# Kernel optimization log

Measured on AMD Instinct MI355X. Metric: run time of the kernel, lower is better.

## Reference

```python
import jax, jax.numpy as jnp
import numpy as np

HEADS = 8  # head_dim = 512 // 8 = 64


def setup_inputs() -> dict:
    key = jax.random.key(0)
    ks = jax.random.split(key, 6)
    B, S, D = 1, 4096, 512
    s = 0.02
    return {
        "hidden_states": jax.random.normal(ks[0], (B, S, D), dtype=jnp.float32),
        "Wq": jax.random.normal(ks[1], (D, D), dtype=jnp.float32) * s,
        "Wk": jax.random.normal(ks[2], (D, D), dtype=jnp.float32) * s,
        "Wv": jax.random.normal(ks[3], (D, D), dtype=jnp.float32) * s,
        "Wo": jax.random.normal(ks[4], (D, D), dtype=jnp.float32) * s,
        "b_out": jnp.zeros((D,), dtype=jnp.float32),
    }


def reference(hidden_states, Wq, Wk, Wv, Wo, b_out):
    B, S, D = hidden_states.shape
    H = HEADS
    hd = D // H
    scale = 1.0 / jnp.sqrt(jnp.asarray(hd, hidden_states.dtype))

    # unfused QKV projections (self-attention, no mask)
    q = hidden_states @ Wq  # [B,S,D]
    k = hidden_states @ Wk
    v = hidden_states @ Wv

    # head_to_batch_dim: [B,S,D] -> [B,H,S,hd]
    def split_heads(t):
        return t.reshape(B, S, H, hd).transpose(0, 2, 1, 3)

    q, k, v = split_heads(q), split_heads(k), split_heads(v)

    # explicit score matrix + softmax (faithful to torch.bmm path)
    scores = jnp.einsum("bhqd,bhkd->bhqk", q, k) * scale  # [B,H,S,S]
    probs = jax.nn.softmax(scores, axis=-1)
    out = jnp.einsum("bhqk,bhkd->bhqd", probs, v)  # [B,H,S,hd]

    # batch_to_head_dim: [B,H,S,hd] -> [B,S,D]
    out = out.transpose(0, 2, 1, 3).reshape(B, S, D)
    # to_out[0] Linear + to_out[1] Dropout (identity at eval)
    return out @ Wo + b_out
```

## Files before the change

kernel.cpp:

```cpp
#include <hip/hip_runtime.h>
#include <hip/hip_bf16.h>

#define S_LEN 4096
#define DMODEL 512
#define NHEADS 8
#define HDIM 64

typedef __hip_bfloat16 bf16;
typedef __attribute__((ext_vector_type(8))) short bf16x8;
typedef __attribute__((ext_vector_type(4))) float f32x4;
typedef __attribute__((ext_vector_type(2))) _Float16 f16x2;
typedef __attribute__((ext_vector_type(4))) _Float16 f16x4;
typedef __attribute__((ext_vector_type(8))) _Float16 f16x8;

__device__ __forceinline__ f32x4 mfma16x16x32(bf16x8 a, bf16x8 b, f32x4 c) {
    return __builtin_amdgcn_mfma_f32_16x16x32_bf16(a, b, c, 0, 0, 0);
}
__device__ __forceinline__ f32x4 mfma16x16x32h(f16x8 a, f16x8 b, f32x4 c) {
    return __builtin_amdgcn_mfma_f32_16x16x32_f16(a, b, c, 0, 0, 0);
}
__device__ __forceinline__ void gload_lds16(const void* g, void* l) {
    __builtin_amdgcn_global_load_lds(
        (const __attribute__((address_space(1))) unsigned int*)g,
        (__attribute__((address_space(3))) unsigned int*)l, 16, 0, 0);
}

__global__ __launch_bounds__(256) void prep(
    const float* __restrict__ X,
    const float* __restrict__ Wq, const float* __restrict__ Wk,
    const float* __restrict__ Wv, const float* __restrict__ Wo,
    bf16* __restrict__ Xb, bf16* __restrict__ Wt)
{
    __shared__ bf16 tile[32][33];
    const int b = blockIdx.x;
    if (b < 1024) {
        int i = (b * 256 + threadIdx.x) * 8;
        float4 a = *(const float4*)(X + i);
        float4 c = *(const float4*)(X + i + 4);
        bf16 tmp[8];
        tmp[0] = __float2bfloat16(a.x); tmp[1] = __float2bfloat16(a.y);
        tmp[2] = __float2bfloat16(a.z); tmp[3] = __float2bfloat16(a.w);
        tmp[4] = __float2bfloat16(c.x); tmp[5] = __float2bfloat16(c.y);
        tmp[6] = __float2bfloat16(c.z); tmp[7] = __float2bfloat16(c.w);
        *(bf16x8*)(Xb + i) = *(bf16x8*)tmp;
    } else {
        const int bb = b - 1024;
        const int z = bb >> 8;
        const int bx = bb & 15, by = (bb >> 4) & 15;
        const float* src = (z == 0) ? Wq : (z == 1) ? Wk : (z == 2) ? Wv : Wo;
        bf16* dst = Wt + (size_t)z * DMODEL * DMODEL;
        const int tx = threadIdx.x & 31, ty = threadIdx.x >> 5;
        const int x = bx * 32 + tx;
        const int y0 = by * 32;
        #pragma unroll
        for (int i = ty; i < 32; i += 8)
            tile[i][tx] = __float2bfloat16(src[(size_t)(y0 + i) * DMODEL + x]);
        __syncthreads();
        const int xo = y0 + tx;
        #pragma unroll
        for (int i = ty; i < 32; i += 8)
            dst[(size_t)(bx * 32 + i) * DMODEL + xo] = tile[tx][i];
    }
}

__global__ __launch_bounds__(256) void gemm_qkv(
    const bf16* __restrict__ A, const bf16* __restrict__ Bt,
    bf16* __restrict__ Qm, bf16* __restrict__ Km, _Float16* __restrict__ Vt)
{
    __shared__ __align__(16) char smem[65536];
    const int m0 = blockIdx.x * 64, n0 = blockIdx.y * 64;
    const int t = threadIdx.x, lane = t & 63, w = t >> 6;
    const int lr = lane & 15, lq = lane >> 4;
    const int swz = (lr & 7) << 4;

    f32x4 acc[3][4];
    #pragma unroll
    for (int i = 0; i < 3; ++i)
        #pragma unroll
        for (int n = 0; n < 4; ++n) acc[i][n] = f32x4{0, 0, 0, 0};

    const int srow = w * 8 + (lane >> 3);
    const int scol = ((lane & 7) ^ (lane >> 3)) * 8;
    const bf16* Ab = A + (size_t)(m0 + srow) * DMODEL + scol;
    const bf16* Bb = Bt + (size_t)(n0 + srow) * DMODEL + scol;

#define QKV_STAGE(k0, b) do {                                                  \
        char* ad = smem + (b) * 8192 + w * 1024;                               \
        gload_lds16(Ab + (k0), ad);                                            \
        gload_lds16(Ab + 32 * DMODEL + (k0), ad + 4096);                       \
        _Pragma("unroll")                                                      \
        for (int mat = 0; mat < 3; ++mat) {                                    \
            char* bd = smem + 16384 + ((b) * 3 + mat) * 8192 + w * 1024;       \
            gload_lds16(Bb + mat * DMODEL * DMODEL + (k0), bd);                \
            gload_lds16(Bb + mat * DMODEL * DMODEL + 32 * DMODEL + (k0), bd + 4096); \
        }                                                                      \
    } while (0)

    QKV_STAGE(0, 0);
    #pragma unroll
    for (int ks = 0; ks < 8; ++ks) {
        const int cur = ks & 1;
        if (ks < 7) {
            QKV_STAGE((ks + 1) * 64, cur ^ 1);
            asm volatile("s_waitcnt vmcnt(8)" ::: "memory");
        } else {
            asm volatile("s_waitcnt vmcnt(0)" ::: "memory");
        }
        __builtin_amdgcn_s_barrier();
        __builtin_amdgcn_sched_barrier(0);
        #pragma unroll
        for (int kc = 0; kc < 2; ++kc) {
            const int co = (kc * 64 + lq * 16) ^ swz;
            bf16x8 a = *(const bf16x8*)(smem + cur * 8192 + (w * 16 + lr) * 128 + co);
            #pragma unroll
            for (int mat = 0; mat < 3; ++mat)
                #pragma unroll
                for (int nt = 0; nt < 4; ++nt) {
                    bf16x8 b = *(const bf16x8*)(smem + 16384 + (cur * 3 + mat) * 8192 +
                                                (nt * 16 + lr) * 128 + co);
                    acc[mat][nt] = mfma16x16x32(a, b, acc[mat][nt]);
                }
        }
        asm volatile("s_waitcnt lgkmcnt(0)" ::: "memory");
        __builtin_amdgcn_sched_barrier(0);
        __builtin_amdgcn_s_barrier();
    }
#undef QKV_STAGE

    bf16*     tbq = (bf16*)smem;
    bf16*     tbk = (bf16*)(smem + 9216);
    _Float16* tbv = (_Float16*)(smem + 18432);
    #pragma unroll
    for (int nt = 0; nt < 4; ++nt)
        #pragma unroll
        for (int r = 0; r < 4; ++r) {
            int row = w * 16 + lq * 4 + r, col = nt * 16 + lr;
            tbq[row * 72 + col] = __float2bfloat16(acc[0][nt][r] * 0.18033688f);
            tbk[row * 72 + col] = __float2bfloat16(acc[1][nt][r]);
            tbv[row * 72 + col] = (_Float16)acc[2][nt][r];
        }
    __syncthreads();
    #pragma unroll
    for (int pass = 0; pass < 2; ++pass) {
        const int m = pass * 32 + (t >> 3), c0 = (t & 7) * 8;
        *(bf16x8*)(Qm + (size_t)(m0 + m) * DMODEL + n0 + c0) =
            *(const bf16x8*)(tbq + m * 72 + c0);
        *(bf16x8*)(Km + (size_t)(m0 + m) * DMODEL + n0 + c0) =
            *(const bf16x8*)(tbk + m * 72 + c0);
    }
    {
        const int c = t >> 2, seg = t & 3;
        _Float16 tmp[16];
        #pragma unroll
        for (int j = 0; j < 16; ++j)
            tmp[j] = tbv[(seg * 16 + j) * 72 + c];
        _Float16* vp = Vt + (size_t)(n0 + c) * S_LEN + m0;
        #pragma unroll
        for (int g = 0; g < 4; ++g) {
            f16x4 vv = {tmp[g * 4 + 0], tmp[g * 4 + 1], tmp[g * 4 + 2], tmp[g * 4 + 3]};
            *(f16x4*)(vp + g * 16 + seg * 4) = vv;
        }
    }
}

__global__ __launch_bounds__(256) void gemm_out(
    const bf16* __restrict__ A, const bf16* __restrict__ Bt,
    float* __restrict__ Out, const float* __restrict__ bias)
{
    __shared__ __align__(16) char smem[32768];
    const int m0 = blockIdx.x * 64, n0 = blockIdx.y * 64;
    const int t = threadIdx.x, lane = t & 63, w = t >> 6;
    const int lr = lane & 15, lq = lane >> 4;
    const int swz = (lr & 7) << 4;

    f32x4 acc[4] = {f32x4{0,0,0,0}, f32x4{0,0,0,0}, f32x4{0,0,0,0}, f32x4{0,0,0,0}};

    const int srow = w * 8 + (lane >> 3);
    const int scol = ((lane & 7) ^ (lane >> 3)) * 8;
    const bf16* Ab = A + (size_t)(m0 + srow) * DMODEL + scol;
    const bf16* Bb = Bt + (size_t)(n0 + srow) * DMODEL + scol;

#define OUT_STAGE(k0, b) do {                                           \
        char* ad = smem + (b) * 8192 + w * 1024;                        \
        char* bd = smem + 16384 + (b) * 8192 + w * 1024;                \
        gload_lds16(Ab + (k0), ad);                                     \
        gload_lds16(Ab + 32 * DMODEL + (k0), ad + 4096);                \
        gload_lds16(Bb + (k0), bd);                                     \
        gload_lds16(Bb + 32 * DMODEL + (k0), bd + 4096);                \
    } while (0)

    OUT_STAGE(0, 0);
    #pragma unroll
    for (int ks = 0; ks < 8; ++ks) {
        const int cur = ks & 1;
        if (ks < 7) {
            OUT_STAGE((ks + 1) * 64, cur ^ 1);
            asm volatile("s_waitcnt vmcnt(4)" ::: "memory");
        } else {
            asm volatile("s_waitcnt vmcnt(0)" ::: "memory");
        }
        __builtin_amdgcn_s_barrier();
        __builtin_amdgcn_sched_barrier(0);
        #pragma unroll
        for (int kc = 0; kc < 2; ++kc) {
            const int co = (kc * 64 + lq * 16) ^ swz;
            bf16x8 a = *(const bf16x8*)(smem + cur * 8192 + (w * 16 + lr) * 128 + co);
            #pragma unroll
            for (int nt = 0; nt < 4; ++nt) {
                bf16x8 b = *(const bf16x8*)(smem + 16384 + cur * 8192 + (nt * 16 + lr) * 128 + co);
                acc[nt] = mfma16x16x32(a, b, acc[nt]);
            }
        }
        asm volatile("s_waitcnt lgkmcnt(0)" ::: "memory");
        __builtin_amdgcn_sched_barrier(0);
        __builtin_amdgcn_s_barrier();
    }
#undef OUT_STAGE

    float* tb = (float*)smem;
    #pragma unroll
    for (int nt = 0; nt < 4; ++nt) {
        const float bv = bias[n0 + nt * 16 + lr];
        #pragma unroll
        for (int r = 0; r < 4; ++r)
            tb[(w * 16 + lq * 4 + r) * 68 + nt * 16 + lr] = acc[nt][r] + bv;
    }
    __syncthreads();
    #pragma unroll
    for (int pass = 0; pass < 2; ++pass) {
        const int m = pass * 32 + (t >> 3), c0 = (t & 7) * 8;
        float4 v0 = *(const float4*)(tb + m * 68 + c0);
        float4 v1 = *(const float4*)(tb + m * 68 + c0 + 4);
        *(float4*)(Out + (size_t)(m0 + m) * DMODEL + n0 + c0) = v0;
        *(float4*)(Out + (size_t)(m0 + m) * DMODEL + n0 + c0 + 4) = v1;
    }
}

__global__ __launch_bounds__(256, 2) void attn_kernel(
    const bf16* __restrict__ Q, const bf16* __restrict__ Kmat,
    const _Float16* __restrict__ Vt, bf16* __restrict__ Oout)
{
    __shared__ __align__(16) char smem[65536];

    const int h = blockIdx.x, qb = blockIdx.y;
    const int t = threadIdx.x, lane = t & 63, w = t >> 6;
    const int lr = lane & 15, lq = lane >> 4;
    const int q0 = qb * 64;

    char* myK = smem + w * 16384;
    char* myV = myK + 8192;

    const int sr = lane >> 3;
    const int scc = (lane & 7) ^ sr;
    const bf16*     gK = Kmat + (size_t)sr * DMODEL + h * HDIM + scc * 8;
    const _Float16* gV = Vt + (size_t)(h * HDIM + sr) * S_LEN + scc * 8;

    bf16x8 qf[4][2];
    #pragma unroll
    for (int qt = 0; qt < 4; ++qt) {
        const bf16* qp = Q + (size_t)(q0 + qt * 16 + lr) * DMODEL + h * HDIM + lq * 8;
        qf[qt][0] = *(const bf16x8*)qp;
        qf[qt][1] = *(const bf16x8*)(qp + 32);
    }

    f32x4 oacc[4][4];
    #pragma unroll
    for (int i = 0; i < 4; ++i)
        #pragma unroll
        for (int j = 0; j < 4; ++j) oacc[i][j] = f32x4{0, 0, 0, 0};
    f32x4 lacc[4];
    #pragma unroll
    for (int i = 0; i < 4; ++i) lacc[i] = f32x4{0, 0, 0, 0};
    const f16x8 vones = {(_Float16)1.0f, (_Float16)1.0f, (_Float16)1.0f, (_Float16)1.0f,
                         (_Float16)1.0f, (_Float16)1.0f, (_Float16)1.0f, (_Float16)1.0f};

    #pragma unroll
    for (int i = 0; i < 8; ++i) {
        gload_lds16(gK + (size_t)(w * 64 + i * 8) * DMODEL, myK + i * 1024);
        gload_lds16(gV + (size_t)(i * 8) * S_LEN + w * 64, myV + i * 1024);
    }

    const int swz = (lr & 7) << 4;

    for (int kt = w; kt < S_LEN / 64; kt += 4) {
        asm volatile("s_waitcnt vmcnt(0)" ::: "memory");

        bf16x8 kf[4][2];
        #pragma unroll
        for (int mt = 0; mt < 4; ++mt) {
            const char* kr = myK + (mt * 16 + lr) * 128;
            kf[mt][0] = *(const bf16x8*)(kr + ((lq * 16) ^ swz));
            kf[mt][1] = *(const bf16x8*)(kr + ((64 + lq * 16) ^ swz));
        }
        f16x8 vA[4], vB[4];
        #pragma unroll
        for (int ht = 0; ht < 4; ++ht) {
            const char* vr = myV + (ht * 16 + lr) * 128;
            vA[ht] = *(const f16x8*)(vr + ((lq * 32) ^ swz));
            vB[ht] = *(const f16x8*)(vr + ((lq * 32 + 16) ^ swz));
        }
        asm volatile("s_waitcnt lgkmcnt(0)" ::: "memory");
        __builtin_amdgcn_sched_barrier(0);

        const int ktn = kt + 4;
        if (ktn < S_LEN / 64) {
            #pragma unroll
            for (int i = 0; i < 8; ++i) {
                gload_lds16(gK + (size_t)(ktn * 64 + i * 8) * DMODEL, myK + i * 1024);
                gload_lds16(gV + (size_t)(i * 8) * S_LEN + ktn * 64, myV + i * 1024);
            }
        }

        __builtin_amdgcn_s_setprio(1);
        f16x4 pf[4][4];
        #pragma unroll
        for (int qt = 0; qt < 4; ++qt) {
            f32x4 st[4];
            #pragma unroll
            for (int mt = 0; mt < 4; ++mt) {
                f32x4 z = {0, 0, 0, 0};
                z = mfma16x16x32(kf[mt][0], qf[qt][0], z);
                z = mfma16x16x32(kf[mt][1], qf[qt][1], z);
                st[mt] = z;
            }
            #pragma unroll
            for (int mt = 0; mt < 4; ++mt) {
                float p0 = __builtin_amdgcn_exp2f(st[mt][0]);
                float p1 = __builtin_amdgcn_exp2f(st[mt][1]);
                float p2 = __builtin_amdgcn_exp2f(st[mt][2]);
                float p3 = __builtin_amdgcn_exp2f(st[mt][3]);
                f16x2 c01 = __builtin_bit_cast(f16x2, __builtin_amdgcn_cvt_pkrtz(p0, p1));
                f16x2 c23 = __builtin_bit_cast(f16x2, __builtin_amdgcn_cvt_pkrtz(p2, p3));
                pf[qt][mt] = __builtin_shufflevector(c01, c23, 0, 1, 2, 3);
            }
        }
        #pragma unroll
        for (int qt = 0; qt < 4; ++qt) {
            f16x8 pp01 = __builtin_shufflevector(pf[qt][0], pf[qt][1], 0, 1, 2, 3, 4, 5, 6, 7);
            f16x8 pp23 = __builtin_shufflevector(pf[qt][2], pf[qt][3], 0, 1, 2, 3, 4, 5, 6, 7);
            #pragma unroll
            for (int ht = 0; ht < 4; ++ht) {
                oacc[qt][ht] = mfma16x16x32h(pp01, vA[ht], oacc[qt][ht]);
                oacc[qt][ht] = mfma16x16x32h(pp23, vB[ht], oacc[qt][ht]);
            }
            lacc[qt] = mfma16x16x32h(pp01, vones, lacc[qt]);
            lacc[qt] = mfma16x16x32h(pp23, vones, lacc[qt]);
        }
        __builtin_amdgcn_s_setprio(0);
    }

    __syncthreads();
    float (*obuf)[3][4][64][4] = (float(*)[3][4][64][4])smem;
    float (*lbuf)[4][16]       = (float(*)[4][16])(smem + 49152);

    #pragma unroll
    for (int qt = 0; qt < 4; ++qt) {
        if (qt != w) {
            int j = qt - (qt > w ? 1 : 0);
            #pragma unroll
            for (int ht = 0; ht < 4; ++ht)
                *(f32x4*)&obuf[w][j][ht][lane][0] = oacc[qt][ht];
        }
    }
    if (lr == 0) {
        #pragma unroll
        for (int qt = 0; qt < 4; ++qt)
            #pragma unroll
            for (int r = 0; r < 4; ++r)
                lbuf[w][qt][lq * 4 + r] = lacc[qt][r];
    }
    __syncthreads();

    f32x4 osum[4];
    #pragma unroll
    for (int qt = 0; qt < 4; ++qt)
        if (qt == w) {
            #pragma unroll
            for (int ht = 0; ht < 4; ++ht) osum[ht] = oacc[qt][ht];
        }
    #pragma unroll
    for (int w2 = 0; w2 < 4; ++w2) {
        if (w2 == w) continue;
        int j = w - (w > w2 ? 1 : 0);
        #pragma unroll
        for (int ht = 0; ht < 4; ++ht)
            osum[ht] += *(const f32x4*)&obuf[w2][j][ht][lane][0];
    }
    float linv[4];
    #pragma unroll
    for (int r = 0; r < 4; ++r) {
        int rr = lq * 4 + r;
        linv[r] = 1.0f / (lbuf[0][w][rr] + lbuf[1][w][rr] + lbuf[2][w][rr] + lbuf[3][w][rr]);
    }
    #pragma unroll
    for (int r = 0; r < 4; ++r) {
        int row = q0 + w * 16 + lq * 4 + r;
        #pragma unroll
        for (int ht = 0; ht < 4; ++ht)
            Oout[(size_t)row * DMODEL + h * HDIM + ht * 16 + lr] =
                __float2bfloat16(osum[ht][r] * linv[r]);
    }
}

extern "C" void kernel_launch(void* const* d_in, const int* in_sizes, int n_in,
                              void* d_out, int out_size, void* d_ws, size_t ws_size,
                              hipStream_t stream) {
    const float* X  = (const float*)d_in[0];
    const float* Wq = (const float*)d_in[1];
    const float* Wk = (const float*)d_in[2];
    const float* Wv = (const float*)d_in[3];
    const float* Wo = (const float*)d_in[4];
    const float* bo = (const float*)d_in[5];
    float* out = (float*)d_out;

    char* ws = (char*)d_ws;
    bf16* Wt = (bf16*)ws;
    bf16* Xb = (bf16*)(ws + (size_t)4 * DMODEL * DMODEL * 2);
    bf16* Qm = Xb + (size_t)S_LEN * DMODEL;
    bf16* Km = Qm + (size_t)S_LEN * DMODEL;
    _Float16* Vt = (_Float16*)(Km + (size_t)S_LEN * DMODEL);
    bf16* AO = (bf16*)(Vt + (size_t)S_LEN * DMODEL);

    bf16* Wot = Wt + (size_t)3 * DMODEL * DMODEL;

    prep<<<2048, 256, 0, stream>>>(X, Wq, Wk, Wv, Wo, Xb, Wt);

    gemm_qkv<<<dim3(S_LEN / 64, DMODEL / 64), 256, 0, stream>>>(
        Xb, Wt, Qm, Km, Vt);

    attn_kernel<<<dim3(NHEADS, S_LEN / 64), 256, 0, stream>>>(Qm, Km, Vt, AO);

    gemm_out<<<dim3(S_LEN / 64, DMODEL / 64), 256, 0, stream>>>(AO, Wot, out, bo);
}
```

Before: 126.7 us.

## Split attention q-tiles across wave pairs sharing K/V LDS staging

The attention block grows from 4 to 8 waves. Each pair of waves shares one K/V LDS buffer, with only the first four waves issuing the global-to-LDS loads. Each wave now handles 2 query tiles instead of 4, which cuts accumulator register pressure and allows more resident waves per CU. The cost is two s_barriers per iteration to coordinate staging and reuse of the shared buffers. The final reduction is reorganized so that each half of the waves combines its partial sums and softmax denominators in LDS.

Measured after the change: 152.6 us. +20.4%, slower.

```diff
diff --git a/kernel.cpp b/kernel.cpp
--- a/kernel.cpp
+++ b/kernel.cpp
@@ -236,7 +236,7 @@
     }
 }
 
-__global__ __launch_bounds__(256, 2) void attn_kernel(
+__global__ __launch_bounds__(512, 4) void attn_kernel(
     const bf16* __restrict__ Q, const bf16* __restrict__ Kmat,
     const _Float16* __restrict__ Vt, bf16* __restrict__ Oout)
 {
@@ -246,8 +246,11 @@
     const int t = threadIdx.x, lane = t & 63, w = t >> 6;
     const int lr = lane & 15, lq = lane >> 4;
     const int q0 = qb * 64;
-
-    char* myK = smem + w * 16384;
+    const int p = w & 3;
+    const bool stager = (w < 4);
+    const int qtbase = stager ? 0 : 2;
+
+    char* myK = smem + p * 16384;
     char* myV = myK + 8192;
 
     const int sr = lane >> 3;
@@ -255,35 +258,38 @@
     const bf16*     gK = Kmat + (size_t)sr * DMODEL + h * HDIM + scc * 8;
     const _Float16* gV = Vt + (size_t)(h * HDIM + sr) * S_LEN + scc * 8;
 
-    bf16x8 qf[4][2];
-    #pragma unroll
-    for (int qt = 0; qt < 4; ++qt) {
-        const bf16* qp = Q + (size_t)(q0 + qt * 16 + lr) * DMODEL + h * HDIM + lq * 8;
-        qf[qt][0] = *(const bf16x8*)qp;
-        qf[qt][1] = *(const bf16x8*)(qp + 32);
-    }
-
-    f32x4 oacc[4][4];
-    #pragma unroll
-    for (int i = 0; i < 4; ++i)
+    bf16x8 qf[2][2];
+    #pragma unroll
+    for (int ql = 0; ql < 2; ++ql) {
+        const bf16* qp = Q + (size_t)(q0 + (qtbase + ql) * 16 + lr) * DMODEL + h * HDIM + lq * 8;
+        qf[ql][0] = *(const bf16x8*)qp;
+        qf[ql][1] = *(const bf16x8*)(qp + 32);
+    }
+
+    f32x4 oacc[2][4];
+    #pragma unroll
+    for (int i = 0; i < 2; ++i)
         #pragma unroll
         for (int j = 0; j < 4; ++j) oacc[i][j] = f32x4{0, 0, 0, 0};
-    f32x4 lacc[4];
-    #pragma unroll
-    for (int i = 0; i < 4; ++i) lacc[i] = f32x4{0, 0, 0, 0};
+    f32x4 lacc[2];
+    lacc[0] = f32x4{0, 0, 0, 0};
+    lacc[1] = f32x4{0, 0, 0, 0};
     const f16x8 vones = {(_Float16)1.0f, (_Float16)1.0f, (_Float16)1.0f, (_Float16)1.0f,
                          (_Float16)1.0f, (_Float16)1.0f, (_Float16)1.0f, (_Float16)1.0f};
 
-    #pragma unroll
-    for (int i = 0; i < 8; ++i) {
-        gload_lds16(gK + (size_t)(w * 64 + i * 8) * DMODEL, myK + i * 1024);
-        gload_lds16(gV + (size_t)(i * 8) * S_LEN + w * 64, myV + i * 1024);
+    if (stager) {
+        #pragma unroll
+        for (int i = 0; i < 8; ++i) {
+            gload_lds16(gK + (size_t)(p * 64 + i * 8) * DMODEL, myK + i * 1024);
+            gload_lds16(gV + (size_t)(i * 8) * S_LEN + p * 64, myV + i * 1024);
+        }
     }
 
     const int swz = (lr & 7) << 4;
 
-    for (int kt = w; kt < S_LEN / 64; kt += 4) {
-        asm volatile("s_waitcnt vmcnt(0)" ::: "memory");
+    for (int kt = p; kt < S_LEN / 64; kt += 4) {
+        if (stager) asm volatile("s_waitcnt vmcnt(0)" ::: "memory");
+        __builtin_amdgcn_s_barrier();
 
         bf16x8 kf[4][2];
         #pragma unroll
@@ -292,35 +298,16 @@
             kf[mt][0] = *(const bf16x8*)(kr + ((lq * 16) ^ swz));
             kf[mt][1] = *(const bf16x8*)(kr + ((64 + lq * 16) ^ swz));
         }
-        f16x8 vA[4], vB[4];
-        #pragma unroll
-        for (int ht = 0; ht < 4; ++ht) {
-            const char* vr = myV + (ht * 16 + lr) * 128;
-            vA[ht] = *(const f16x8*)(vr + ((lq * 32) ^ swz));
-            vB[ht] = *(const f16x8*)(vr + ((lq * 32 + 16) ^ swz));
-        }
-        asm volatile("s_waitcnt lgkmcnt(0)" ::: "memory");
-        __builtin_amdgcn_sched_barrier(0);
-
-        const int ktn = kt + 4;
-        if (ktn < S_LEN / 64) {
-            #pragma unroll
-            for (int i = 0; i < 8; ++i) {
-                gload_lds16(gK + (size_t)(ktn * 64 + i * 8) * DMODEL, myK + i * 1024);
-                gload_lds16(gV + (size_t)(i * 8) * S_LEN + ktn * 64, myV + i * 1024);
-            }
-        }
-
-        __builtin_amdgcn_s_setprio(1);
-        f16x4 pf[4][4];
-        #pragma unroll
-        for (int qt = 0; qt < 4; ++qt) {
+
+        f16x4 pf[2][4];
+        #pragma unroll
+        for (int ql = 0; ql < 2; ++ql) {
             f32x4 st[4];
             #pragma unroll
             for (int mt = 0; mt < 4; ++mt) {
                 f32x4 z = {0, 0, 0, 0};
-                z = mfma16x16x32(kf[mt][0], qf[qt][0], z);
-                z = mfma16x16x32(kf[mt][1], qf[qt][1], z);
+                z = mfma16x16x32(kf[mt][0], qf[ql][0], z);
+                z = mfma16x16x32(kf[mt][1], qf[ql][1], z);
                 st[mt] = z;
             }
             #pragma unroll
@@ -331,74 +318,97 @@
                 float p3 = __builtin_amdgcn_exp2f(st[mt][3]);
                 f16x2 c01 = __builtin_bit_cast(f16x2, __builtin_amdgcn_cvt_pkrtz(p0, p1));
                 f16x2 c23 = __builtin_bit_cast(f16x2, __builtin_amdgcn_cvt_pkrtz(p2, p3));
-                pf[qt][mt] = __builtin_shufflevector(c01, c23, 0, 1, 2, 3);
+                pf[ql][mt] = __builtin_shufflevector(c01, c23, 0, 1, 2, 3);
             }
         }
-        #pragma unroll
-        for (int qt = 0; qt < 4; ++qt) {
-            f16x8 pp01 = __builtin_shufflevector(pf[qt][0], pf[qt][1], 0, 1, 2, 3, 4, 5, 6, 7);
-            f16x8 pp23 = __builtin_shufflevector(pf[qt][2], pf[qt][3], 0, 1, 2, 3, 4, 5, 6, 7);
+
+        f16x8 vA[4], vB[4];
+        #pragma unroll
+        for (int ht = 0; ht < 4; ++ht) {
+            const char* vr = myV + (ht * 16 + lr) * 128;
+            vA[ht] = *(const f16x8*)(vr + ((lq * 32) ^ swz));
+            vB[ht] = *(const f16x8*)(vr + ((lq * 32 + 16) ^ swz));
+        }
+        asm volatile("s_waitcnt lgkmcnt(0)" ::: "memory");
+        __builtin_amdgcn_sched_barrier(0);
+        __builtin_amdgcn_s_barrier();
+
+        const int ktn = kt + 4;
+        if (stager && ktn < S_LEN / 64) {
+            #pragma unroll
+            for (int i = 0; i < 8; ++i) {
+                gload_lds16(gK + (size_t)(ktn * 64 + i * 8) * DMODEL, myK + i * 1024);
+                gload_lds16(gV + (size_t)(i * 8) * S_LEN + ktn * 64, myV + i * 1024);
+            }
+        }
+
+        __builtin_amdgcn_s_setprio(1);
+        #pragma unroll
+        for (int ql = 0; ql < 2; ++ql) {
+            f16x8 pp01 = __builtin_shufflevector(pf[ql][0], pf[ql][1], 0, 1, 2, 3, 4, 5, 6, 7);
+            f16x8 pp23 = __builtin_shufflevector(pf[ql][2], pf[ql][3], 0, 1, 2, 3, 4, 5, 6, 7);
             #pragma unroll
             for (int ht = 0; ht < 4; ++ht) {
-                oacc[qt][ht] = mfma16x16x32h(pp01, vA[ht], oacc[qt][ht]);
-                oacc[qt][ht] = mfma16x16x32h(pp23, vB[ht], oacc[qt][ht]);
+                oacc[ql][ht] = mfma16x16x32h(pp01, vA[ht], oacc[ql][ht]);
+                oacc[ql][ht] = mfma16x16x32h(pp23, vB[ht], oacc[ql][ht]);
             }
-            lacc[qt] = mfma16x16x32h(pp01, vones, lacc[qt]);
-            lacc[qt] = mfma16x16x32h(pp23, vones, lacc[qt]);
+            lacc[ql] = mfma16x16x32h(pp01, vones, lacc[ql]);
+            lacc[ql] = mfma16x16x32h(pp23, vones, lacc[ql]);
         }
         __builtin_amdgcn_s_setprio(0);
     }
 
+    float (*obuf)[2][4][64][4] = (float(*)[2][4][64][4])smem;
+    float (*lbuf)[2][16]       = (float(*)[2][16])smem;
+
+    const bool fin = ((w & 2) == 0);
+    #pragma unroll
+    for (int ql = 0; ql < 2; ++ql) {
+        if (!(fin && ql == (w & 1))) {
+            #pragma unroll
+            for (int ht = 0; ht < 4; ++ht)
+                *(f32x4*)&obuf[w][ql][ht][lane][0] = oacc[ql][ht];
+        }
+    }
+    if (lr == 0) {
+        #pragma unroll
+        for (int ql = 0; ql < 2; ++ql)
+            #pragma unroll
+            for (int r = 0; r < 4; ++r)
+                lbuf[w][ql][lq * 4 + r] = lacc[ql][r];
+    }
     __syncthreads();
-    float (*obuf)[3][4][64][4] = (float(*)[3][4][64][4])smem;
-    float (*lbuf)[4][16]       = (float(*)[4][16])(smem + 49152);
-
-    #pragma unroll
-    for (int qt = 0; qt < 4; ++qt) {
-        if (qt != w) {
-            int j = qt - (qt > w ? 1 : 0);
+
+    if (fin) {
+        const int ql = w & 1;
+        const int qtg = qtbase + ql;
+        const int wq = w & 4;
+        f32x4 osum[4];
+        #pragma unroll
+        for (int ht = 0; ht < 4; ++ht) osum[ht] = oacc[ql][ht];
+        #pragma unroll
+        for (int i = 0; i < 4; ++i) {
+            const int w2 = wq + i;
+            if (w2 == w) continue;
             #pragma unroll
             for (int ht = 0; ht < 4; ++ht)
-                *(f32x4*)&obuf[w][j][ht][lane][0] = oacc[qt][ht];
-        }
-    }
-    if (lr == 0) {
-        #pragma unroll
-        for (int qt = 0; qt < 4; ++qt)
-            #pragma unroll
-            for (int r = 0; r < 4; ++r)
-                lbuf[w][qt][lq * 4 + r] = lacc[qt][r];
-    }
-    __syncthreads();
-
-    f32x4 osum[4];
-    #pragma unroll
-    for (int qt = 0; qt < 4; ++qt)
-        if (qt == w) {
-            #pragma unroll
-            for (int ht = 0; ht < 4; ++ht) osum[ht] = oacc[qt][ht];
-        }
-    #pragma unroll
-    for (int w2 = 0; w2 < 4; ++w2) {
-        if (w2 == w) continue;
-        int j = w - (w > w2 ? 1 : 0);
-        #pragma unroll
-        for (int ht = 0; ht < 4; ++ht)
-            osum[ht] += *(const f32x4*)&obuf[w2][j][ht][lane][0];
-    }
-    float linv[4];
-    #pragma unroll
-    for (int r = 0; r < 4; ++r) {
-        int rr = lq * 4 + r;
-        linv[r] = 1.0f / (lbuf[0][w][rr] + lbuf[1][w][rr] + lbuf[2][w][rr] + lbuf[3][w][rr]);
-    }
-    #pragma unroll
-    for (int r = 0; r < 4; ++r) {
-        int row = q0 + w * 16 + lq * 4 + r;
-        #pragma unroll
-        for (int ht = 0; ht < 4; ++ht)
-            Oout[(size_t)row * DMODEL + h * HDIM + ht * 16 + lr] =
-                __float2bfloat16(osum[ht][r] * linv[r]);
+                osum[ht] += *(const f32x4*)&obuf[w2][ql][ht][lane][0];
+        }
+        float linv[4];
+        #pragma unroll
+        for (int r = 0; r < 4; ++r) {
+            const int rr = lq * 4 + r;
+            linv[r] = 1.0f / (lbuf[wq][ql][rr] + lbuf[wq + 1][ql][rr] +
+                              lbuf[wq + 2][ql][rr] + lbuf[wq + 3][ql][rr]);
+        }
+        #pragma unroll
+        for (int r = 0; r < 4; ++r) {
+            const int row = q0 + qtg * 16 + lq * 4 + r;
+            #pragma unroll
+            for (int ht = 0; ht < 4; ++ht)
+                Oout[(size_t)row * DMODEL + h * HDIM + ht * 16 + lr] =
+                    __float2bfloat16(osum[ht][r] * linv[r]);
+        }
     }
 }
 
@@ -428,7 +438,7 @@
     gemm_qkv<<<dim3(S_LEN / 64, DMODEL / 64), 256, 0, stream>>>(
         Xb, Wt, Qm, Km, Vt);
 
-    attn_kernel<<<dim3(NHEADS, S_LEN / 64), 256, 0, stream>>>(Qm, Km, Vt, AO);
+    attn_kernel<<<dim3(NHEADS, S_LEN / 64), 512, 0, stream>>>(Qm, Km, Vt, AO);
 
     gemm_out<<<dim3(S_LEN / 64, DMODEL / 64), 256, 0, stream>>>(AO, Wot, out, bo);
 }
```
